# Kernel optimization log

Hardware: AMD Instinct MI355X
Metric: run time of the kernel (lower is better)

The kernel has to match this reference:

```python
import jax, jax.numpy as jnp
import numpy as np

ARITY = 4
DEPTH = 8          # leaves = ARITY**DEPTH = 65536; internal nodes = (4**8-1)//3 = 21845
IN_DIM = 64
MEM = 128
HID = 128


def setup_inputs() -> dict:
    key = jax.random.key(0)
    ks = jax.random.split(key, 20)
    n_leaves = ARITY ** DEPTH
    n_internal = (ARITY ** DEPTH - 1) // (ARITY - 1)
    s = 0.05
    inp = {
        "inputs": jax.random.normal(ks[0], (n_leaves, IN_DIM), jnp.float32),
        "ops": jax.random.randint(ks[1], (n_internal,), 0, 2, jnp.int32),
        # MLP (all bias-free); torch Linear weight layout [out, in]
        "W1": jax.random.normal(ks[2], (MEM, IN_DIM), jnp.float32) * s,
        "W2": jax.random.normal(ks[3], (3 * MEM, MEM), jnp.float32) * s,
        "W3": jax.random.normal(ks[4], (2 * MEM, 3 * MEM), jnp.float32) * s,
        "Wp": jax.random.normal(ks[5], (MEM, 2 * MEM), jnp.float32) * s,
        # ChildSumTreeRNN
        "Wand": jax.random.normal(ks[6], (MEM, MEM), jnp.float32) * s,
        "Wor": jax.random.normal(ks[7], (MEM, MEM), jnp.float32) * s,
        "Rw1": jax.random.normal(ks[8], (HID, MEM), jnp.float32) * s,
        "Rb1": jnp.zeros((HID,), jnp.float32),
        "Rw2": jax.random.normal(ks[9], (HID, HID), jnp.float32) * s,
        "Rb2": jnp.zeros((HID,), jnp.float32),
        "Rw3": jax.random.normal(ks[10], (HID, HID), jnp.float32) * s,
        "Rb3": jnp.zeros((HID,), jnp.float32),
        "Rwp": jax.random.normal(ks[11], (1, HID), jnp.float32) * s,
        "Rbp": jnp.zeros((1,), jnp.float32),
    }
    return inp


def reference(inputs, ops, W1, W2, W3, Wp, Wand, Wor,
              Rw1, Rb1, Rw2, Rb2, Rw3, Rb3, Rwp, Rbp):
    # MLP embedding of all leaves  [n_leaves, MEM]
    h = jnp.tanh(inputs @ W1.T)
    h = jnp.tanh(h @ W2.T)
    h = jnp.tanh(h @ W3.T)
    h = jnp.tanh(h @ Wp.T)

    # ChildSumTreeRNN, level by level (children before parents).
    # Complete arity-4 tree: level l has 4**l internal nodes; ops is
    # level-ordered from the root, so level l starts at (4**l - 1)//3.
    for l in range(DEPTH - 1, -1, -1):
        n = ARITY ** l
        start = (ARITY ** l - 1) // (ARITY - 1)
        ops_l = ops[start:start + n]                      # [n]
        ch = h.reshape(n, ARITY, MEM)                     # children states
        ha = jnp.tanh(jnp.einsum('ncm,om->nco', ch, Wand)).mean(axis=1)
        ho = jnp.tanh(jnp.einsum('ncm,om->nco', ch, Wor)).mean(axis=1)
        h = jnp.where((ops_l == 0)[:, None], ha, ho)      # [n, MEM]

    x = jax.nn.relu(h @ Rw1.T + Rb1)
    x = jax.nn.relu(x @ Rw2.T + Rb2)
    x = jax.nn.relu(x @ Rw3.T + Rb3)
    out = x @ Rwp.T + Rbp                                 # [1, 1]
    return out
```

## Files before the change

kernel.cpp:

```cpp
#include <hip/hip_runtime.h>
#include <hip/hip_bf16.h>
#include <stdint.h>

#define N_LEAVES 65536
#define MEM 128
#define HID 128

typedef float  f32x4 __attribute__((ext_vector_type(4)));
typedef short  s16x8 __attribute__((ext_vector_type(8)));
typedef unsigned short u16;
typedef u16    u16x8 __attribute__((ext_vector_type(8)));

__device__ __forceinline__ u16 f2bf(float x) {
    unsigned u = __builtin_bit_cast(unsigned, x);
    u += 0x7FFFu + ((u >> 16) & 1u);
    return (u16)(u >> 16);
}
__device__ __forceinline__ float bf2f(u16 b) {
    unsigned u = ((unsigned)b) << 16;
    return __builtin_bit_cast(float, u);
}
__device__ __forceinline__ float hif(float x) {
    return __builtin_bit_cast(float, __builtin_bit_cast(unsigned, x) & 0xffff0000u);
}
__device__ __forceinline__ unsigned packbf(float e0, float e1) {
    return __builtin_amdgcn_perm(__builtin_bit_cast(unsigned, e1),
                                 __builtin_bit_cast(unsigned, e0), 0x07060302u);
}
__device__ __forceinline__ float tanh_c(float x) {
    float E = __builtin_amdgcn_exp2f(x * 2.8853900817779268f);
    return 1.0f - 2.0f * __builtin_amdgcn_rcpf(E + 1.0f);
}
__device__ __forceinline__ float tanh_p(float x) {
    float x2 = x * x;
    float poly = x * (1.0f + x2 * (-0.33333334f + x2 * 0.13333334f));
    float E = __builtin_amdgcn_exp2f(x * 2.8853900817779268f);
    float ex = 1.0f - 2.0f * __builtin_amdgcn_rcpf(E + 1.0f);
    return (__builtin_fabsf(x) < 0.25f) ? poly : ex;
}

__device__ __forceinline__ f32x4 mfma_bf(s16x8 a, s16x8 b, f32x4 c) {
    return __builtin_amdgcn_mfma_f32_16x16x32_bf16(a, b, c, 0, 0, 0);
}

__global__ __launch_bounds__(256) void prep_all(
    const float* __restrict__ W1, const float* __restrict__ W2,
    const float* __restrict__ W3, const float* __restrict__ Wp,
    const float* __restrict__ Wand, const float* __restrict__ Wor,
    u16* __restrict__ w1tH, u16* __restrict__ w1tL,
    u16* __restrict__ w2tH, u16* __restrict__ w2tL,
    u16* __restrict__ w3tH, u16* __restrict__ w3tL,
    u16* __restrict__ wptH, u16* __restrict__ wptL,
    u16* __restrict__ waH,  u16* __restrict__ waL,
    u16* __restrict__ woH,  u16* __restrict__ woL)
{
    int g = blockIdx.x * 256 + threadIdx.x;
    const float* W; u16 *Th, *Tl; int K, N, base;
    if (g < 1024)       { W = W1;  Th = w1tH; Tl = w1tL; N = 128; K = 64;  base = 0; }
    else if (g < 7168)  { W = W2;  Th = w2tH; Tl = w2tL; N = 384; K = 128; base = 1024; }
    else if (g < 19456) { W = W3;  Th = w3tH; Tl = w3tL; N = 256; K = 384; base = 7168; }
    else if (g < 23552) { W = Wp;  Th = wptH; Tl = wptL; N = 128; K = 256; base = 19456; }
    else if (g < 25600) { W = Wand; Th = waH; Tl = waL;  N = 128; K = 128; base = 23552; }
    else if (g < 27648) { W = Wor;  Th = woH; Tl = woL;  N = 128; K = 128; base = 25600; }
    else return;
    int t = g - base;
    int kg8 = K >> 3;
    int n = t / kg8, kg = t - n * kg8;
    const float* src = &W[(size_t)n * K + kg * 8];
    size_t dst = ((size_t)kg * N + n) * 8;
    u16x8 hv, lv;
    #pragma unroll
    for (int j = 0; j < 8; ++j) {
        float v = src[j];
        u16 hb = f2bf(v);
        hv[j] = hb;
        lv[j] = f2bf(v - bf2f(hb));
    }
    *(u16x8*)&Th[dst] = hv;
    *(u16x8*)&Tl[dst] = lv;
}

__device__ __forceinline__ int act_g(int Wu, int row, int c4) {
    return row * (Wu >> 3) + (c4 ^ (row & 7));
}

template<int FJ, int KTN, int WIN, int WOUT>
__device__ __forceinline__ void mlp_layer_t(
    const u16* inH, const u16* inL,
    const u16* __restrict__ BtH, const u16* __restrict__ BtL,
    u16* outH, u16* outL,
    int w, int l)
{
    const int lr = l & 15, lc = l >> 4;
    const int featBase = w * (FJ * 16);

    f32x4 acc[FJ][2] = {};
    s16x8 wh[2][FJ], wl[2][FJ];

    #pragma unroll
    for (int fi = 0; fi < FJ; ++fi) {
        int o = (lc * WOUT + featBase + fi * 16 + lr) * 8;
        wh[0][fi] = *(const s16x8*)&BtH[o];
        wl[0][fi] = *(const s16x8*)&BtL[o];
    }

    #pragma unroll
    for (int kt = 0; kt < KTN; ++kt) {
        const int cur = kt & 1;
        if (kt + 1 < KTN) {
            #pragma unroll
            for (int fi = 0; fi < FJ; ++fi) {
                int o = (((kt + 1) * 4 + lc) * WOUT + featBase + fi * 16 + lr) * 8;
                wh[cur ^ 1][fi] = *(const s16x8*)&BtH[o];
                wl[cur ^ 1][fi] = *(const s16x8*)&BtL[o];
            }
        }
        s16x8 ah[2], al[2];
        #pragma unroll
        for (int rj = 0; rj < 2; ++rj) {
            int off = act_g(WIN, rj * 16 + lr, kt * 4 + lc) * 8;
            ah[rj] = *(const s16x8*)&inH[off];
            al[rj] = *(const s16x8*)&inL[off];
        }
        #pragma unroll
        for (int fi = 0; fi < FJ; ++fi)
            #pragma unroll
            for (int rj = 0; rj < 2; ++rj) {
                f32x4 a = acc[fi][rj];
                a = mfma_bf(wh[cur][fi], ah[rj], a);
                a = mfma_bf(wh[cur][fi], al[rj], a);
                a = mfma_bf(wl[cur][fi], ah[rj], a);
                acc[fi][rj] = a;
            }
    }

    #pragma unroll
    for (int fi = 0; fi < FJ; ++fi)
        #pragma unroll
        for (int rj = 0; rj < 2; ++rj) {
            int m  = rj * 16 + lr;
            int n0 = featBase + fi * 16 + lc * 4;
            f32x4 v = acc[fi][rj];
            float t0 = tanh_c(v[0]), t1 = tanh_c(v[1]);
            float t2 = tanh_c(v[2]), t3 = tanh_c(v[3]);
            uint2 hp, lp;
            hp.x = packbf(t0, t1);
            hp.y = packbf(t2, t3);
            lp.x = packbf(t0 - hif(t0), t1 - hif(t1));
            lp.y = packbf(t2 - hif(t2), t3 - hif(t3));
            int go = act_g(WOUT, m, n0 >> 3) * 8 + (n0 & 7);
            *(uint2*)&outH[go] = hp;
            *(uint2*)&outL[go] = lp;
        }
}

template<int CJ, int FJ, bool TOGLOBAL>
__device__ __forceinline__ void tree_level(
    const u16* inH, const u16* inL,
    const u16* __restrict__ wAH, const u16* __restrict__ wAL,
    const u16* __restrict__ wOH, const u16* __restrict__ wOL,
    const int* __restrict__ opsL,
    u16* outH, u16* outL,
    int outRowBase, int nValid, int cfBase, int ffBase, int l)
{
    const int lr = l & 15, lc = l >> 4;
    f32x4 accA[CJ][FJ] = {};
    f32x4 accO[CJ][FJ] = {};

    #pragma unroll
    for (int kt = 0; kt < 4; ++kt) {
        s16x8 ah[CJ], al[CJ];
        #pragma unroll
        for (int c = 0; c < CJ; ++c) {
            int off = act_g(128, (cfBase + c) * 16 + lr, kt * 4 + lc) * 8;
            ah[c] = *(const s16x8*)&inH[off];
            al[c] = *(const s16x8*)&inL[off];
        }
        #pragma unroll
        for (int f = 0; f < FJ; ++f) {
            int wo = ((kt * 4 + lc) * 128 + ffBase + f * 16 + lr) * 8;
            s16x8 bah = *(const s16x8*)&wAH[wo];
            s16x8 bal = *(const s16x8*)&wAL[wo];
            s16x8 boh = *(const s16x8*)&wOH[wo];
            s16x8 bol = *(const s16x8*)&wOL[wo];
            #pragma unroll
            for (int c = 0; c < CJ; ++c) {
                f32x4 a = accA[c][f];
                a = mfma_bf(ah[c], bah, a);
                a = mfma_bf(ah[c], bal, a);
                a = mfma_bf(al[c], bah, a);
                accA[c][f] = a;
                f32x4 o = accO[c][f];
                o = mfma_bf(ah[c], boh, o);
                o = mfma_bf(ah[c], bol, o);
                o = mfma_bf(al[c], boh, o);
                accO[c][f] = o;
            }
        }
    }

    #pragma unroll
    for (int c = 0; c < CJ; ++c) {
        int p = (cfBase + c) * 4 + lc;
        if (p < nValid) {
            int op = opsL[p];
            #pragma unroll
            for (int f = 0; f < FJ; ++f) {
                f32x4 v = op ? accO[c][f] : accA[c][f];
                float t = 0.25f * (tanh_p(v[0]) + tanh_p(v[1]) + tanh_p(v[2]) + tanh_p(v[3]));
                unsigned bits = __builtin_bit_cast(unsigned, t);
                u16 hb = (u16)(bits >> 16);
                float lof = t - __builtin_bit_cast(float, bits & 0xffff0000u);
                u16 lb = (u16)(__builtin_bit_cast(unsigned, lof) >> 16);
                int feat = ffBase + f * 16 + lr;
                if constexpr (TOGLOBAL) {
                    int ga = (outRowBase + p) * 128 + feat;
                    outH[ga] = hb;
                    outL[ga] = lb;
                } else {
                    int go = act_g(128, outRowBase + p, feat >> 3) * 8 + (feat & 7);
                    outH[go] = hb;
                    outL[go] = lb;
                }
            }
        }
    }
}

__global__ __launch_bounds__(512, 4) void leaf_fused(
    const float* __restrict__ x,
    const u16* __restrict__ W1tH, const u16* __restrict__ W1tL,
    const u16* __restrict__ W2tH, const u16* __restrict__ W2tL,
    const u16* __restrict__ W3tH, const u16* __restrict__ W3tL,
    const u16* __restrict__ WptH, const u16* __restrict__ WptL,
    const u16* __restrict__ waH,  const u16* __restrict__ waL,
    const u16* __restrict__ woH,  const u16* __restrict__ woL,
    const int* __restrict__ ops,
    u16* __restrict__ l7H, u16* __restrict__ l7L)
{
    __shared__ u16 buf0[2 * 32 * 384];
    __shared__ u16 buf1[2 * 32 * 256];

    const int tid = threadIdx.x;
    const int w = tid >> 6, l = tid & 63;
    const int blk = blockIdx.x;
    const int rowBase = blk * 32;

    if (tid < 256) {
        int row = tid >> 3;
        int c0  = (tid & 7) * 8;
        const float* src = &x[(size_t)(rowBase + row) * 64 + c0];
        float4 v0 = *(const float4*)src;
        float4 v1 = *(const float4*)(src + 4);
        float xs[8] = {v0.x, v0.y, v0.z, v0.w, v1.x, v1.y, v1.z, v1.w};
        int go = act_g(64, row, c0 >> 3) * 8;
        uint4 hp, lp;
        hp.x = packbf(xs[0], xs[1]); hp.y = packbf(xs[2], xs[3]);
        hp.z = packbf(xs[4], xs[5]); hp.w = packbf(xs[6], xs[7]);
        lp.x = packbf(xs[0] - hif(xs[0]), xs[1] - hif(xs[1]));
        lp.y = packbf(xs[2] - hif(xs[2]), xs[3] - hif(xs[3]));
        lp.z = packbf(xs[4] - hif(xs[4]), xs[5] - hif(xs[5]));
        lp.w = packbf(xs[6] - hif(xs[6]), xs[7] - hif(xs[7]));
        *(uint4*)&buf0[go] = hp;
        *(uint4*)&buf0[32 * 64 + go] = lp;
    }
    __syncthreads();

    mlp_layer_t<1, 2, 64, 128>(buf0, buf0 + 32 * 64, W1tH, W1tL,
                               buf1, buf1 + 32 * 128, w, l);
    __syncthreads();
    mlp_layer_t<3, 4, 128, 384>(buf1, buf1 + 32 * 128, W2tH, W2tL,
                                buf0, buf0 + 32 * 384, w, l);
    __syncthreads();
    mlp_layer_t<2, 12, 384, 256>(buf0, buf0 + 32 * 384, W3tH, W3tL,
                                 buf1, buf1 + 32 * 256, w, l);
    __syncthreads();
    mlp_layer_t<1, 8, 256, 128>(buf1, buf1 + 32 * 256, WptH, WptL,
                                buf0, buf0 + 32 * 128, w, l);
    __syncthreads();
    tree_level<2, 1, true>(buf0, buf0 + 32 * 128, waH, waL, woH, woL,
                           ops + 5461 + blk * 8, l7H, l7L,
                           blk * 8, 8, 0, w * 16, l);
}

__global__ __launch_bounds__(512, 4) void tree3(
    const u16* __restrict__ inH, const u16* __restrict__ inL,
    const u16* __restrict__ wAH, const u16* __restrict__ wAL,
    const u16* __restrict__ wOH, const u16* __restrict__ wOL,
    const int* __restrict__ ops0, const int* __restrict__ ops1,
    const int* __restrict__ ops2,
    u16* __restrict__ outH, u16* __restrict__ outL)
{
    __shared__ u16 L0H[16384], L0L[16384];
    __shared__ u16 L1H[4096],  L1L[4096];

    const int tid = threadIdx.x;
    const int w = tid >> 6, l = tid & 63;
    const int blk = blockIdx.x;

    #pragma unroll
    for (int it = 0; it < 4; ++it) {
        int g = tid + it * 512;
        int row = g >> 4, c4 = g & 15;
        size_t src = (size_t)(blk * 128 + row) * 128 + c4 * 8;
        int dst = act_g(128, row, c4) * 8;
        *(u16x8*)&L0H[dst] = *(const u16x8*)&inH[src];
        *(u16x8*)&L0L[dst] = *(const u16x8*)&inL[src];
    }
    __syncthreads();

    tree_level<2, 4, false>(L0H, L0L, wAH, wAL, wOH, wOL, ops0 + blk * 32,
                            L1H, L1L, 0, 32, (w & 3) * 2, (w >> 2) * 64, l);
    __syncthreads();
    tree_level<1, 2, false>(L1H, L1L, wAH, wAL, wOH, wOL, ops1 + blk * 8,
                            L0H, L0L, 0, 8, (w >> 2), (w & 3) * 32, l);
    __syncthreads();
    tree_level<1, 1, true>(L0H, L0L, wAH, wAL, wOH, wOL, ops2 + blk * 2,
                           outH, outL, blk * 2, 2, 0, w * 16, l);
}

__global__ __launch_bounds__(512) void tree_tail(
    const u16* __restrict__ l4H, const u16* __restrict__ l4L,
    const int* __restrict__ ops,
    const u16* __restrict__ wAH, const u16* __restrict__ wAL,
    const u16* __restrict__ wOH, const u16* __restrict__ wOL,
    const float* __restrict__ Rw1, const float* __restrict__ Rb1,
    const float* __restrict__ Rw2, const float* __restrict__ Rb2,
    const float* __restrict__ Rw3, const float* __restrict__ Rb3,
    const float* __restrict__ Rwp, const float* __restrict__ Rbp,
    float* __restrict__ out)
{
    __shared__ u16 LH[16384], LL[16384];
    __shared__ u16 OH[8192],  OL[8192];
    __shared__ float F[4 * 128];

    const int tid = threadIdx.x;
    const int w = tid >> 6, l = tid & 63;

    #pragma unroll
    for (int it = 0; it < 4; ++it) {
        int g = tid + it * 512;
        int row = g >> 4, c4 = g & 15;
        size_t src = (size_t)row * 128 + c4 * 8;
        int dst = act_g(128, row, c4) * 8;
        *(u16x8*)&LH[dst] = *(const u16x8*)&l4H[src];
        *(u16x8*)&LL[dst] = *(const u16x8*)&l4L[src];
    }
    __syncthreads();
    tree_level<1, 8, false>(LH, LL, wAH, wAL, wOH, wOL, ops + 21,
                            OH, OL, 0, 32, w, 0, l);
    __syncthreads();

    #pragma unroll
    for (int it = 0; it < 4; ++it) {
        int g = tid + it * 512;
        int row = g >> 4, c4 = g & 15;
        size_t src = (size_t)(128 + row) * 128 + c4 * 8;
        int dst = act_g(128, row, c4) * 8;
        *(u16x8*)&LH[dst] = *(const u16x8*)&l4H[src];
        *(u16x8*)&LL[dst] = *(const u16x8*)&l4L[src];
    }
    __syncthreads();
    tree_level<1, 8, false>(LH, LL, wAH, wAL, wOH, wOL, ops + 21 + 32,
                            OH, OL, 32, 32, w, 0, l);
    __syncthreads();

    tree_level<1, 4, false>(OH, OL, wAH, wAL, wOH, wOL, ops + 5,
                            LH, LL, 0, 16, (w & 3), (w >> 2) * 64, l);
    __syncthreads();

    tree_level<1, 1, false>(LH, LL, wAH, wAL, wOH, wOL, ops + 1,
                            OH, OL, 0, 4, 0, w * 16, l);
    __syncthreads();

    tree_level<1, 1, false>(OH, OL, wAH, wAL, wOH, wOL, ops + 0,
                            LH, LL, 0, 1, 0, w * 16, l);
    __syncthreads();

    if (tid < 128) F[tid] = bf2f(LH[tid]) + bf2f(LL[tid]);
    __syncthreads();
    if (tid < 128) {
        const float4* wr = (const float4*)&Rw1[tid * 128];
        const float4* xr = (const float4*)&F[0];
        float s = 0;
        for (int m = 0; m < 32; ++m) {
            float4 wv = wr[m], xv = xr[m];
            s += wv.x*xv.x + wv.y*xv.y + wv.z*xv.z + wv.w*xv.w;
        }
        F[128 + tid] = fmaxf(s + Rb1[tid], 0.f);
    }
    __syncthreads();
    if (tid < 128) {
        const float4* wr = (const float4*)&Rw2[tid * 128];
        const float4* xr = (const float4*)&F[128];
        float s = 0;
        for (int m = 0; m < 32; ++m) {
            float4 wv = wr[m], xv = xr[m];
            s += wv.x*xv.x + wv.y*xv.y + wv.z*xv.z + wv.w*xv.w;
        }
        F[256 + tid] = fmaxf(s + Rb2[tid], 0.f);
    }
    __syncthreads();
    if (tid < 128) {
        const float4* wr = (const float4*)&Rw3[tid * 128];
        const float4* xr = (const float4*)&F[256];
        float s = 0;
        for (int m = 0; m < 32; ++m) {
            float4 wv = wr[m], xv = xr[m];
            s += wv.x*xv.x + wv.y*xv.y + wv.z*xv.z + wv.w*xv.w;
        }
        F[384 + tid] = fmaxf(s + Rb3[tid], 0.f) * Rwp[tid];
    }
    __syncthreads();
    if (tid == 0) {
        float t = 0.f;
        for (int i = 0; i < 128; ++i) t += F[384 + i];
        out[0] = t + Rbp[0];
    }
}

extern "C" void kernel_launch(void* const* d_in, const int* in_sizes, int n_in,
                              void* d_out, int out_size, void* d_ws, size_t ws_size,
                              hipStream_t stream)
{
    const float* inputs = (const float*)d_in[0];
    const int*   ops    = (const int*)d_in[1];
    const float* W1     = (const float*)d_in[2];
    const float* W2     = (const float*)d_in[3];
    const float* W3     = (const float*)d_in[4];
    const float* Wp     = (const float*)d_in[5];
    const float* Wand   = (const float*)d_in[6];
    const float* Wor    = (const float*)d_in[7];
    const float* Rw1    = (const float*)d_in[8];
    const float* Rb1    = (const float*)d_in[9];
    const float* Rw2    = (const float*)d_in[10];
    const float* Rb2    = (const float*)d_in[11];
    const float* Rw3    = (const float*)d_in[12];
    const float* Rb3    = (const float*)d_in[13];
    const float* Rwp    = (const float*)d_in[14];
    const float* Rbp    = (const float*)d_in[15];
    float* out = (float*)d_out;
    u16* ws = (u16*)d_ws;

    size_t off = 0;
    u16* w1tH = ws + off; off += 8192;   u16* w1tL = ws + off; off += 8192;
    u16* w2tH = ws + off; off += 49152;  u16* w2tL = ws + off; off += 49152;
    u16* w3tH = ws + off; off += 98304;  u16* w3tL = ws + off; off += 98304;
    u16* wptH = ws + off; off += 32768;  u16* wptL = ws + off; off += 32768;
    u16* waH  = ws + off; off += 16384;  u16* waL  = ws + off; off += 16384;
    u16* woH  = ws + off; off += 16384;  u16* woL  = ws + off; off += 16384;
    u16* l7H  = ws + off; off += (size_t)16384 * 128;
    u16* l7L  = ws + off; off += (size_t)16384 * 128;
    u16* l4H  = ws + off; off += 256 * 128;
    u16* l4L  = ws + off; off += 256 * 128;

    prep_all<<<108, 256, 0, stream>>>(W1, W2, W3, Wp, Wand, Wor,
        w1tH, w1tL, w2tH, w2tL, w3tH, w3tL, wptH, wptL, waH, waL, woH, woL);

    leaf_fused<<<N_LEAVES / 32, 512, 0, stream>>>(
        inputs, w1tH, w1tL, w2tH, w2tL, w3tH, w3tL, wptH, wptL,
        waH, waL, woH, woL, ops, l7H, l7L);

    tree3<<<128, 512, 0, stream>>>(l7H, l7L, waH, waL, woH, woL,
        ops + 1365, ops + 341, ops + 85, l4H, l4L);

    tree_tail<<<1, 512, 0, stream>>>(l4H, l4L, ops, waH, waL, woH, woL,
        Rw1, Rb1, Rw2, Rb2, Rw3, Rb3, Rwp, Rbp, out);
}
```

Measured before the change: 162.3 us.

## Double leaf MLP row tile to 64 and split tree tail across kernels

The leaf MLP kernel now processes 64 rows per block instead of 32. Each wave computes four 16-row tiles, so every weight fragment feeds more MFMAs. Weights get a triple-buffered register prefetch and activations a double-buffered one, and launch bounds drop to one block per SM so the larger register set fits. The single-block tree tail is replaced by a 2-block tree3 launch plus a small fp32 root and regressor kernel, spreading the top tree levels across more CUs. This trades occupancy for more reuse and adds one kernel launch.

```diff
diff --git a/kernel.cpp b/kernel.cpp
--- a/kernel.cpp
+++ b/kernel.cpp
@@ -93,51 +93,63 @@
 {
     const int lr = l & 15, lc = l >> 4;
     const int featBase = w * (FJ * 16);
-
-    f32x4 acc[FJ][2] = {};
-    s16x8 wh[2][FJ], wl[2][FJ];
-
-    #pragma unroll
-    for (int fi = 0; fi < FJ; ++fi) {
-        int o = (lc * WOUT + featBase + fi * 16 + lr) * 8;
-        wh[0][fi] = *(const s16x8*)&BtH[o];
-        wl[0][fi] = *(const s16x8*)&BtL[o];
+    constexpr int D = (KTN < 3) ? KTN : 3;
+
+    f32x4 acc[FJ][4] = {};
+    s16x8 wh[D][FJ], wl[D][FJ];
+    s16x8 ah[2][4], al[2][4];
+
+    #pragma unroll
+    for (int d = 0; d < D; ++d)
+        #pragma unroll
+        for (int fi = 0; fi < FJ; ++fi) {
+            int o = ((d * 4 + lc) * WOUT + featBase + fi * 16 + lr) * 8;
+            wh[d][fi] = *(const s16x8*)&BtH[o];
+            wl[d][fi] = *(const s16x8*)&BtL[o];
+        }
+    #pragma unroll
+    for (int rj = 0; rj < 4; ++rj) {
+        int off = act_g(WIN, rj * 16 + lr, lc) * 8;
+        ah[0][rj] = *(const s16x8*)&inH[off];
+        al[0][rj] = *(const s16x8*)&inL[off];
     }
 
     #pragma unroll
     for (int kt = 0; kt < KTN; ++kt) {
-        const int cur = kt & 1;
+        const int ws_ = kt % D;
+        const int as_ = kt & 1;
         if (kt + 1 < KTN) {
             #pragma unroll
-            for (int fi = 0; fi < FJ; ++fi) {
-                int o = (((kt + 1) * 4 + lc) * WOUT + featBase + fi * 16 + lr) * 8;
-                wh[cur ^ 1][fi] = *(const s16x8*)&BtH[o];
-                wl[cur ^ 1][fi] = *(const s16x8*)&BtL[o];
+            for (int rj = 0; rj < 4; ++rj) {
+                int off = act_g(WIN, rj * 16 + lr, (kt + 1) * 4 + lc) * 8;
+                ah[as_ ^ 1][rj] = *(const s16x8*)&inH[off];
+                al[as_ ^ 1][rj] = *(const s16x8*)&inL[off];
             }
-        }
-        s16x8 ah[2], al[2];
-        #pragma unroll
-        for (int rj = 0; rj < 2; ++rj) {
-            int off = act_g(WIN, rj * 16 + lr, kt * 4 + lc) * 8;
-            ah[rj] = *(const s16x8*)&inH[off];
-            al[rj] = *(const s16x8*)&inL[off];
         }
         #pragma unroll
         for (int fi = 0; fi < FJ; ++fi)
             #pragma unroll
-            for (int rj = 0; rj < 2; ++rj) {
+            for (int rj = 0; rj < 4; ++rj) {
                 f32x4 a = acc[fi][rj];
-                a = mfma_bf(wh[cur][fi], ah[rj], a);
-                a = mfma_bf(wh[cur][fi], al[rj], a);
-                a = mfma_bf(wl[cur][fi], ah[rj], a);
+                a = mfma_bf(wh[ws_][fi], ah[as_][rj], a);
+                a = mfma_bf(wh[ws_][fi], al[as_][rj], a);
+                a = mfma_bf(wl[ws_][fi], ah[as_][rj], a);
                 acc[fi][rj] = a;
             }
+        if (kt + D < KTN) {
+            #pragma unroll
+            for (int fi = 0; fi < FJ; ++fi) {
+                int o = (((kt + D) * 4 + lc) * WOUT + featBase + fi * 16 + lr) * 8;
+                wh[ws_][fi] = *(const s16x8*)&BtH[o];
+                wl[ws_][fi] = *(const s16x8*)&BtL[o];
+            }
+        }
     }
 
     #pragma unroll
     for (int fi = 0; fi < FJ; ++fi)
         #pragma unroll
-        for (int rj = 0; rj < 2; ++rj) {
+        for (int rj = 0; rj < 4; ++rj) {
             int m  = rj * 16 + lr;
             int n0 = featBase + fi * 16 + lc * 4;
             f32x4 v = acc[fi][rj];
@@ -227,7 +239,7 @@
     }
 }
 
-__global__ __launch_bounds__(512, 4) void leaf_fused(
+__global__ __launch_bounds__(512, 1) void leaf_fused(
     const float* __restrict__ x,
     const u16* __restrict__ W1tH, const u16* __restrict__ W1tL,
     const u16* __restrict__ W2tH, const u16* __restrict__ W2tL,
@@ -238,15 +250,15 @@
     const int* __restrict__ ops,
     u16* __restrict__ l7H, u16* __restrict__ l7L)
 {
-    __shared__ u16 buf0[2 * 32 * 384];
-    __shared__ u16 buf1[2 * 32 * 256];
+    __shared__ u16 bufA[49152];
+    __shared__ u16 bufB[32768];
 
     const int tid = threadIdx.x;
     const int w = tid >> 6, l = tid & 63;
     const int blk = blockIdx.x;
-    const int rowBase = blk * 32;
-
-    if (tid < 256) {
+    const int rowBase = blk * 64;
+
+    {
         int row = tid >> 3;
         int c0  = (tid & 7) * 8;
         const float* src = &x[(size_t)(rowBase + row) * 64 + c0];
@@ -261,26 +273,26 @@
         lp.y = packbf(xs[2] - hif(xs[2]), xs[3] - hif(xs[3]));
         lp.z = packbf(xs[4] - hif(xs[4]), xs[5] - hif(xs[5]));
         lp.w = packbf(xs[6] - hif(xs[6]), xs[7] - hif(xs[7]));
-        *(uint4*)&buf0[go] = hp;
-        *(uint4*)&buf0[32 * 64 + go] = lp;
-    }
-    __syncthreads();
-
-    mlp_layer_t<1, 2, 64, 128>(buf0, buf0 + 32 * 64, W1tH, W1tL,
-                               buf1, buf1 + 32 * 128, w, l);
-    __syncthreads();
-    mlp_layer_t<3, 4, 128, 384>(buf1, buf1 + 32 * 128, W2tH, W2tL,
-                                buf0, buf0 + 32 * 384, w, l);
-    __syncthreads();
-    mlp_layer_t<2, 12, 384, 256>(buf0, buf0 + 32 * 384, W3tH, W3tL,
-                                 buf1, buf1 + 32 * 256, w, l);
-    __syncthreads();
-    mlp_layer_t<1, 8, 256, 128>(buf1, buf1 + 32 * 256, WptH, WptL,
-                                buf0, buf0 + 32 * 128, w, l);
-    __syncthreads();
-    tree_level<2, 1, true>(buf0, buf0 + 32 * 128, waH, waL, woH, woL,
-                           ops + 5461 + blk * 8, l7H, l7L,
-                           blk * 8, 8, 0, w * 16, l);
+        *(uint4*)&bufB[go] = hp;
+        *(uint4*)&bufB[4096 + go] = lp;
+    }
+    __syncthreads();
+
+    mlp_layer_t<1, 2, 64, 128>(bufB, bufB + 4096, W1tH, W1tL,
+                               bufB + 8192, bufB + 16384, w, l);
+    __syncthreads();
+    mlp_layer_t<3, 4, 128, 384>(bufB + 8192, bufB + 16384, W2tH, W2tL,
+                                bufA, bufA + 24576, w, l);
+    __syncthreads();
+    mlp_layer_t<2, 12, 384, 256>(bufA, bufA + 24576, W3tH, W3tL,
+                                 bufB, bufB + 16384, w, l);
+    __syncthreads();
+    mlp_layer_t<1, 8, 256, 128>(bufB, bufB + 16384, WptH, WptL,
+                                bufA, bufA + 8192, w, l);
+    __syncthreads();
+    tree_level<1, 4, true>(bufA, bufA + 8192, waH, waL, woH, woL,
+                           ops + 5461 + blk * 16, l7H, l7L,
+                           blk * 16, 16, (w >> 1), (w & 1) * 64, l);
 }
 
 __global__ __launch_bounds__(512, 4) void tree3(
@@ -319,100 +331,79 @@
                            outH, outL, blk * 2, 2, 0, w * 16, l);
 }
 
-__global__ __launch_bounds__(512) void tree_tail(
-    const u16* __restrict__ l4H, const u16* __restrict__ l4L,
+__global__ __launch_bounds__(128) void tail_final(
+    const u16* __restrict__ l1H, const u16* __restrict__ l1L,
     const int* __restrict__ ops,
-    const u16* __restrict__ wAH, const u16* __restrict__ wAL,
-    const u16* __restrict__ wOH, const u16* __restrict__ wOL,
+    const float* __restrict__ Wand, const float* __restrict__ Wor,
     const float* __restrict__ Rw1, const float* __restrict__ Rb1,
     const float* __restrict__ Rw2, const float* __restrict__ Rb2,
     const float* __restrict__ Rw3, const float* __restrict__ Rb3,
     const float* __restrict__ Rwp, const float* __restrict__ Rbp,
     float* __restrict__ out)
 {
-    __shared__ u16 LH[16384], LL[16384];
-    __shared__ u16 OH[8192],  OL[8192];
-    __shared__ float F[4 * 128];
-
-    const int tid = threadIdx.x;
-    const int w = tid >> 6, l = tid & 63;
-
-    #pragma unroll
-    for (int it = 0; it < 4; ++it) {
-        int g = tid + it * 512;
-        int row = g >> 4, c4 = g & 15;
-        size_t src = (size_t)row * 128 + c4 * 8;
-        int dst = act_g(128, row, c4) * 8;
-        *(u16x8*)&LH[dst] = *(const u16x8*)&l4H[src];
-        *(u16x8*)&LL[dst] = *(const u16x8*)&l4L[src];
-    }
-    __syncthreads();
-    tree_level<1, 8, false>(LH, LL, wAH, wAL, wOH, wOL, ops + 21,
-                            OH, OL, 0, 32, w, 0, l);
-    __syncthreads();
-
-    #pragma unroll
-    for (int it = 0; it < 4; ++it) {
-        int g = tid + it * 512;
-        int row = g >> 4, c4 = g & 15;
-        size_t src = (size_t)(128 + row) * 128 + c4 * 8;
-        int dst = act_g(128, row, c4) * 8;
-        *(u16x8*)&LH[dst] = *(const u16x8*)&l4H[src];
-        *(u16x8*)&LL[dst] = *(const u16x8*)&l4L[src];
-    }
-    __syncthreads();
-    tree_level<1, 8, false>(LH, LL, wAH, wAL, wOH, wOL, ops + 21 + 32,
-                            OH, OL, 32, 32, w, 0, l);
-    __syncthreads();
-
-    tree_level<1, 4, false>(OH, OL, wAH, wAL, wOH, wOL, ops + 5,
-                            LH, LL, 0, 16, (w & 3), (w >> 2) * 64, l);
-    __syncthreads();
-
-    tree_level<1, 1, false>(LH, LL, wAH, wAL, wOH, wOL, ops + 1,
-                            OH, OL, 0, 4, 0, w * 16, l);
-    __syncthreads();
-
-    tree_level<1, 1, false>(OH, OL, wAH, wAL, wOH, wOL, ops + 0,
-                            LH, LL, 0, 1, 0, w * 16, l);
-    __syncthreads();
-
-    if (tid < 128) F[tid] = bf2f(LH[tid]) + bf2f(LL[tid]);
-    __syncthreads();
-    if (tid < 128) {
-        const float4* wr = (const float4*)&Rw1[tid * 128];
+    __shared__ float h[512];
+    __shared__ float F[512];
+    const int o = threadIdx.x;
+
+    for (int i = o; i < 512; i += 128) h[i] = bf2f(l1H[i]) + bf2f(l1L[i]);
+    __syncthreads();
+
+    {
+        const float* Wsel = (ops[0] == 0) ? Wand : Wor;
+        const float4* wr = (const float4*)&Wsel[o * 128];
+        const float4* h0 = (const float4*)&h[0];
+        const float4* h1 = (const float4*)&h[128];
+        const float4* h2 = (const float4*)&h[256];
+        const float4* h3 = (const float4*)&h[384];
+        float s0 = 0, s1 = 0, s2 = 0, s3 = 0;
+        for (int m = 0; m < 32; ++m) {
+            float4 wv = wr[m];
+            float4 a0 = h0[m], a1 = h1[m], a2 = h2[m], a3 = h3[m];
+            s0 += wv.x*a0.x + wv.y*a0.y + wv.z*a0.z + wv.w*a0.w;
+            s1 += wv.x*a1.x + wv.y*a1.y + wv.z*a1.z + wv.w*a1.w;
+            s2 += wv.x*a2.x + wv.y*a2.y + wv.z*a2.z + wv.w*a2.w;
+            s3 += wv.x*a3.x + wv.y*a3.y + wv.z*a3.z + wv.w*a3.w;
+        }
+        F[o] = 0.25f * (tanh_p(s0) + tanh_p(s1) + tanh_p(s2) + tanh_p(s3));
+    }
+    __syncthreads();
+    {
+        const float4* wr = (const float4*)&Rw1[o * 128];
         const float4* xr = (const float4*)&F[0];
         float s = 0;
         for (int m = 0; m < 32; ++m) {
             float4 wv = wr[m], xv = xr[m];
             s += wv.x*xv.x + wv.y*xv.y + wv.z*xv.z + wv.w*xv.w;
         }
-        F[128 + tid] = fmaxf(s + Rb1[tid], 0.f);
-    }
-    __syncthreads();
-    if (tid < 128) {
-        const float4* wr = (const float4*)&Rw2[tid * 128];
+        __syncthreads();
+        F[128 + o] = fmaxf(s + Rb1[o], 0.f);
+    }
+    __syncthreads();
+    {
+        const float4* wr = (const float4*)&Rw2[o * 128];
         const float4* xr = (const float4*)&F[128];
         float s = 0;
         for (int m = 0; m < 32; ++m) {
             float4 wv = wr[m], xv = xr[m];
             s += wv.x*xv.x + wv.y*xv.y + wv.z*xv.z + wv.w*xv.w;
         }
-        F[256 + tid] = fmaxf(s + Rb2[tid], 0.f);
-    }
-    __syncthreads();
-    if (tid < 128) {
-        const float4* wr = (const float4*)&Rw3[tid * 128];
+        __syncthreads();
+        F[256 + o] = fmaxf(s + Rb2[o], 0.f);
+    }
+    __syncthreads();
+    {
+        const float4* wr = (const float4*)&Rw3[o * 128];
         const float4* xr = (const float4*)&F[256];
         float s = 0;
         for (int m = 0; m < 32; ++m) {
             float4 wv = wr[m], xv = xr[m];
             s += wv.x*xv.x + wv.y*xv.y + wv.z*xv.z + wv.w*xv.w;
         }
-        F[384 + tid] = fmaxf(s + Rb3[tid], 0.f) * Rwp[tid];
-    }
-    __syncthreads();
-    if (tid == 0) {
+        __syncthreads();
+        F[384 + o] = fmaxf(s + Rb3[o], 0.f) * Rwp[o];
+    }
+    __syncthreads();
+    if (o == 0) {
         float t = 0.f;
         for (int i = 0; i < 128; ++i) t += F[384 + i];
         out[0] = t + Rbp[0];
@@ -453,17 +444,22 @@
     u16* l7L  = ws + off; off += (size_t)16384 * 128;
     u16* l4H  = ws + off; off += 256 * 128;
     u16* l4L  = ws + off; off += 256 * 128;
+    u16* l1H  = ws + off; off += 512;
+    u16* l1L  = ws + off; off += 512;
 
     prep_all<<<108, 256, 0, stream>>>(W1, W2, W3, Wp, Wand, Wor,
         w1tH, w1tL, w2tH, w2tL, w3tH, w3tL, wptH, wptL, waH, waL, woH, woL);
 
-    leaf_fused<<<N_LEAVES / 32, 512, 0, stream>>>(
+    leaf_fused<<<N_LEAVES / 64, 512, 0, stream>>>(
         inputs, w1tH, w1tL, w2tH, w2tL, w3tH, w3tL, wptH, wptL,
         waH, waL, woH, woL, ops, l7H, l7L);
 
     tree3<<<128, 512, 0, stream>>>(l7H, l7L, waH, waL, woH, woL,
         ops + 1365, ops + 341, ops + 85, l4H, l4L);
 
-    tree_tail<<<1, 512, 0, stream>>>(l4H, l4L, ops, waH, waL, woH, woL,
+    tree3<<<2, 512, 0, stream>>>(l4H, l4L, waH, waL, woH, woL,
+        ops + 21, ops + 5, ops + 1, l1H, l1L);
+
+    tail_final<<<1, 128, 0, stream>>>(l1H, l1L, ops, Wand, Wor,
         Rw1, Rb1, Rw2, Rb2, Rw3, Rb3, Rwp, Rbp, out);
 }
```

Result: faster. 143.0 us (-11.9%).
